# Performance work log

Hardware: AMD Instinct MI355X
Metric: run time of the kernel (lower is better)

The kernel has to match this reference:

```python
import jax, jax.numpy as jnp
import numpy as np

N, F, F1 = 8192, 256, 64
EDGE_PROB = 0.01  # adjacency density


def setup_inputs() -> dict:
    key = jax.random.key(0)
    kX, kA, kW, ka = jax.random.split(key, 4)
    X = jax.random.normal(kX, (N, F), dtype=jnp.float32)
    # binary adjacency mask (float, as in the original where A multiplies the -1e10 mask)
    A = (jax.random.uniform(kA, (N, N)) < EDGE_PROB).astype(jnp.float32)
    # glorot_uniform init for W [F1, F] and a [2, F1, 1]
    limW = float(np.sqrt(6.0 / (F1 + F)))
    W = jax.random.uniform(kW, (F1, F), minval=-limW, maxval=limW, dtype=jnp.float32)
    lima = float(np.sqrt(6.0 / (F1 + 1)))
    a = jax.random.uniform(ka, (2, F1, 1), minval=-lima, maxval=lima, dtype=jnp.float32)
    return {"X": X, "A": A, "W": W, "a": a}


def reference(X, A, W, a):
    x_features = X @ W.T                       # [N, F1]
    att_self = x_features @ a[0]               # [N, 1]
    att_neighbours = x_features @ a[1]         # [N, 1]
    att = att_self + att_neighbours.T          # [N, N] broadcast additive score
    att = jnp.where(att > 0, att, 0.2 * att)   # LeakyReLU(alpha=0.2)
    att_masked = att + (-1e10) * (1.0 - A)     # mask non-edges
    dense = jax.nn.softmax(att_masked, axis=0) # column-wise softmax (axis=0, as in source)
    return dense @ x_features                  # [N, F1]
```

## Files before the change

kernel.cpp:

```cpp
#include <hip/hip_runtime.h>
#include <math.h>

#define NN   8192
#define FF   256
#define FF1  64
#define CAP  256
#define RREP 32

__global__ __launch_bounds__(256) void k1_feat(const float* __restrict__ X,
                                               const float* __restrict__ W,
                                               const float* __restrict__ a,
                                               float* __restrict__ xf,
                                               float* __restrict__ s,
                                               float* __restrict__ t,
                                               float* __restrict__ D_rep) {
    __shared__ float Xs[32 * FF];
    const int tid  = threadIdx.x;
    const int row0 = blockIdx.x * 32;

    {
        const int gid = blockIdx.x * 256 + tid;
        ((float4*)D_rep)[gid] = make_float4(0.f, 0.f, 0.f, 0.f);
    }

    const float4* Xg  = (const float4*)(X + (size_t)row0 * FF);
    float4*       Xs4 = (float4*)Xs;
#pragma unroll
    for (int v = 0; v < 8; ++v) Xs4[tid + v * 256] = Xg[tid + v * 256];
    __syncthreads();

    const int f  = tid & 63;
    const int rg = tid >> 6;

    float acc[8] = {0.f,0.f,0.f,0.f,0.f,0.f,0.f,0.f};
    const float4* Wrow = (const float4*)(W + (size_t)f * FF);
    for (int k4 = 0; k4 < FF / 4; ++k4) {
        float4 wv = Wrow[k4];
#pragma unroll
        for (int r = 0; r < 8; ++r) {
            float4 xv = *(const float4*)&Xs[(rg * 8 + r) * FF + k4 * 4];
            acc[r] = fmaf(wv.x, xv.x, acc[r]);
            acc[r] = fmaf(wv.y, xv.y, acc[r]);
            acc[r] = fmaf(wv.z, xv.z, acc[r]);
            acc[r] = fmaf(wv.w, xv.w, acc[r]);
        }
    }

    const float a0 = a[f];
    const float a1 = a[FF1 + f];
#pragma unroll
    for (int r = 0; r < 8; ++r) {
        const int row = row0 + rg * 8 + r;
        xf[(size_t)row * FF1 + f] = acc[r];
        float vs = acc[r] * a0;
        float vt = acc[r] * a1;
#pragma unroll
        for (int off = 32; off; off >>= 1) {
            vs += __shfl_xor(vs, off);
            vt += __shfl_xor(vt, off);
        }
        if (f == 0) { s[row] = vs; t[row] = vt; }
    }
}

__global__ __launch_bounds__(256) void k2_scan(const float* __restrict__ A,
                                               unsigned short* __restrict__ idx,
                                               int* __restrict__ counts) {
    const int tid  = threadIdx.x;
    const int lane = tid & 63;
    const int wv   = tid >> 6;
    __shared__ unsigned short lbuf[256 * 8];
    __shared__ int wtot[4];

    for (int r = 0; r < 4; ++r) {
        const int i = blockIdx.x * 4 + r;
        int c = 0;
        const float4* Arow = (const float4*)(A + (size_t)i * NN);
#pragma unroll
        for (int k = 0; k < 8; ++k) {
            const int v = tid + k * 256;
            float4 av = Arow[v];
            if (av.x != 0.f) { lbuf[tid * 8 + (c & 7)] = (unsigned short)(4 * v + 0); ++c; }
            if (av.y != 0.f) { lbuf[tid * 8 + (c & 7)] = (unsigned short)(4 * v + 1); ++c; }
            if (av.z != 0.f) { lbuf[tid * 8 + (c & 7)] = (unsigned short)(4 * v + 2); ++c; }
            if (av.w != 0.f) { lbuf[tid * 8 + (c & 7)] = (unsigned short)(4 * v + 3); ++c; }
        }
        if (c > 8) c = 8;

        int sc = c;
#pragma unroll
        for (int off = 1; off < 64; off <<= 1) {
            int n = __shfl_up(sc, off);
            if (lane >= off) sc += n;
        }
        if (lane == 63) wtot[wv] = sc;
        __syncthreads();

        int base = sc - c;
#pragma unroll
        for (int w = 0; w < 4; ++w) if (w < wv) base += wtot[w];

        for (int q = 0; q < c; ++q) {
            const int pos = base + q;
            if (pos < CAP) idx[(size_t)i * CAP + pos] = lbuf[tid * 8 + q];
        }
        if (tid == 255) {
            const int total = base + c;
            counts[i] = (total < CAP) ? total : CAP;
        }
        __syncthreads();
    }
}

__global__ __launch_bounds__(256) void k2b_edge(const float* __restrict__ s,
                                                const float* __restrict__ t,
                                                const unsigned short* __restrict__ idx,
                                                const int* __restrict__ counts,
                                                float* __restrict__ ev,
                                                float* __restrict__ D_rep) {
    const int wv   = threadIdx.x >> 6;
    const int lane = threadIdx.x & 63;
    const int i    = blockIdx.x * 4 + wv;
    float* __restrict__ Dr = D_rep + (size_t)(blockIdx.x & (RREP - 1)) * NN;

    const int   cnt = counts[i];
    const float si  = s[i];
    for (int p = lane; p < cnt; p += 64) {
        const int j = idx[(size_t)i * CAP + p];
        const float x  = si + t[j];
        const float lr = x > 0.f ? x : 0.2f * x;
        const float e  = __expf(lr);
        ev[(size_t)i * CAP + p] = e;
        unsafeAtomicAdd(&Dr[j], e);
    }
}

__global__ __launch_bounds__(256) void k2c_yf(const float* __restrict__ D_rep,
                                              const float* __restrict__ xf,
                                              float* __restrict__ yf) {
    const int wv   = threadIdx.x >> 6;
    const int lane = threadIdx.x & 63;
    const int j    = blockIdx.x * 4 + wv;

    float d = (lane < RREP) ? D_rep[(size_t)lane * NN + j] : 0.f;
#pragma unroll
    for (int off = 16; off; off >>= 1) d += __shfl_xor(d, off);
    d = __shfl(d, 0);
    const float rD = 1.0f / d;
    yf[(size_t)j * FF1 + lane] = xf[(size_t)j * FF1 + lane] * rD;
}

__global__ __launch_bounds__(256) void k3_apply(const float* __restrict__ yf,
                                                const unsigned short* __restrict__ idx,
                                                const float* __restrict__ ev,
                                                const int* __restrict__ counts,
                                                float* __restrict__ out) {
    const int wave = threadIdx.x >> 6;
    const int lane = threadIdx.x & 63;
    const int i    = blockIdx.x * 4 + wave;

    const int cnt = counts[i];
    float acc0 = 0.f, acc1 = 0.f, acc2 = 0.f, acc3 = 0.f;

    for (int base = 0; base < cnt; base += 64) {
        const int p = base + lane;
        const bool act = (p < cnt);
        int   j = act ? (int)idx[(size_t)i * CAP + p] : 0;
        float w = act ? ev[(size_t)i * CAP + p] : 0.f;

#pragma unroll
        for (int e = 0; e < 64; e += 4) {
            {
                const int   je = __builtin_amdgcn_readlane(j, e + 0);
                const float we = __int_as_float(__builtin_amdgcn_readlane(__float_as_int(w), e + 0));
                acc0 = fmaf(we, yf[(size_t)je * FF1 + lane], acc0);
            }
            {
                const int   je = __builtin_amdgcn_readlane(j, e + 1);
                const float we = __int_as_float(__builtin_amdgcn_readlane(__float_as_int(w), e + 1));
                acc1 = fmaf(we, yf[(size_t)je * FF1 + lane], acc1);
            }
            {
                const int   je = __builtin_amdgcn_readlane(j, e + 2);
                const float we = __int_as_float(__builtin_amdgcn_readlane(__float_as_int(w), e + 2));
                acc2 = fmaf(we, yf[(size_t)je * FF1 + lane], acc2);
            }
            {
                const int   je = __builtin_amdgcn_readlane(j, e + 3);
                const float we = __int_as_float(__builtin_amdgcn_readlane(__float_as_int(w), e + 3));
                acc3 = fmaf(we, yf[(size_t)je * FF1 + lane], acc3);
            }
        }
    }
    out[(size_t)i * FF1 + lane] = (acc0 + acc1) + (acc2 + acc3);
}

extern "C" void kernel_launch(void* const* d_in, const int* in_sizes, int n_in,
                              void* d_out, int out_size, void* d_ws, size_t ws_size,
                              hipStream_t stream) {
    const float* X = (const float*)d_in[0];
    const float* A = (const float*)d_in[1];
    const float* W = (const float*)d_in[2];
    const float* a = (const float*)d_in[3];
    float* out = (float*)d_out;

    char* ws = (char*)d_ws;
    float* xf = (float*)ws;                                  ws += (size_t)NN * FF1 * 4;
    float* yf = (float*)ws;                                  ws += (size_t)NN * FF1 * 4;
    float* s  = (float*)ws;                                  ws += (size_t)NN * 4;
    float* t  = (float*)ws;                                  ws += (size_t)NN * 4;
    int*   counts = (int*)ws;                                ws += (size_t)NN * 4;
    unsigned short* idx = (unsigned short*)ws;               ws += (size_t)NN * CAP * 2;
    float* ev = (float*)ws;                                  ws += (size_t)NN * CAP * 4;
    float* D_rep = (float*)ws;

    k1_feat<<<NN / 32, 256, 0, stream>>>(X, W, a, xf, s, t, D_rep);
    k2_scan<<<NN / 4, 256, 0, stream>>>(A, idx, counts);
    k2b_edge<<<NN / 4, 256, 0, stream>>>(s, t, idx, counts, ev, D_rep);
    k2c_yf<<<NN / 4, 256, 0, stream>>>(D_rep, xf, yf);
    k3_apply<<<NN / 4, 256, 0, stream>>>(yf, idx, ev, counts, out);
}
```

Before: 109.7 us.

## Merge feature GEMM and adjacency scan into one heterogeneous launch; skip empty chunks

Combines the X@W feature kernel and the adjacency-row scan into a single launch whose blocks branch by blockIdx. The feature part is re-tiled to 8 rows per block (1024 blocks) so it can run alongside the bandwidth-bound scan blocks. This removes one launch and the serialization between two independent stages. The apply kernel also skips 16-edge readlane chunks beyond the neighbour count, avoiding wasted gathers from padded lanes. The merged kernel carries the shared-memory footprint of both paths and has lower register reuse per feature row.

After: 119.6 us. +9.0%, slower.

```diff
diff --git a/kernel.cpp b/kernel.cpp
--- a/kernel.cpp
+++ b/kernel.cpp
@@ -6,109 +6,103 @@
 #define FF1  64
 #define CAP  256
 #define RREP 32
-
-__global__ __launch_bounds__(256) void k1_feat(const float* __restrict__ X,
-                                               const float* __restrict__ W,
-                                               const float* __restrict__ a,
-                                               float* __restrict__ xf,
-                                               float* __restrict__ s,
-                                               float* __restrict__ t,
-                                               float* __restrict__ D_rep) {
-    __shared__ float Xs[32 * FF];
-    const int tid  = threadIdx.x;
-    const int row0 = blockIdx.x * 32;
-
-    {
-        const int gid = blockIdx.x * 256 + tid;
-        ((float4*)D_rep)[gid] = make_float4(0.f, 0.f, 0.f, 0.f);
-    }
-
-    const float4* Xg  = (const float4*)(X + (size_t)row0 * FF);
-    float4*       Xs4 = (float4*)Xs;
-#pragma unroll
-    for (int v = 0; v < 8; ++v) Xs4[tid + v * 256] = Xg[tid + v * 256];
-    __syncthreads();
-
-    const int f  = tid & 63;
-    const int rg = tid >> 6;
-
-    float acc[8] = {0.f,0.f,0.f,0.f,0.f,0.f,0.f,0.f};
-    const float4* Wrow = (const float4*)(W + (size_t)f * FF);
-    for (int k4 = 0; k4 < FF / 4; ++k4) {
-        float4 wv = Wrow[k4];
-#pragma unroll
-        for (int r = 0; r < 8; ++r) {
-            float4 xv = *(const float4*)&Xs[(rg * 8 + r) * FF + k4 * 4];
-            acc[r] = fmaf(wv.x, xv.x, acc[r]);
-            acc[r] = fmaf(wv.y, xv.y, acc[r]);
-            acc[r] = fmaf(wv.z, xv.z, acc[r]);
-            acc[r] = fmaf(wv.w, xv.w, acc[r]);
-        }
-    }
-
-    const float a0 = a[f];
-    const float a1 = a[FF1 + f];
-#pragma unroll
-    for (int r = 0; r < 8; ++r) {
-        const int row = row0 + rg * 8 + r;
-        xf[(size_t)row * FF1 + f] = acc[r];
-        float vs = acc[r] * a0;
-        float vt = acc[r] * a1;
-#pragma unroll
-        for (int off = 32; off; off >>= 1) {
-            vs += __shfl_xor(vs, off);
-            vt += __shfl_xor(vt, off);
-        }
-        if (f == 0) { s[row] = vs; t[row] = vt; }
-    }
-}
-
-__global__ __launch_bounds__(256) void k2_scan(const float* __restrict__ A,
-                                               unsigned short* __restrict__ idx,
-                                               int* __restrict__ counts) {
+#define K1B  1024
+#define SCB  2048
+
+__global__ __launch_bounds__(256) void kA(const float* __restrict__ X,
+                                          const float* __restrict__ A,
+                                          const float* __restrict__ W,
+                                          const float* __restrict__ a,
+                                          float* __restrict__ xf,
+                                          float* __restrict__ s,
+                                          float* __restrict__ t,
+                                          float* __restrict__ D_rep,
+                                          unsigned short* __restrict__ idx,
+                                          int* __restrict__ counts) {
+    __shared__ float          Xs[8 * FF];
+    __shared__ unsigned short lbuf[256 * 8];
+    __shared__ int            wtot[4];
+
     const int tid  = threadIdx.x;
     const int lane = tid & 63;
     const int wv   = tid >> 6;
-    __shared__ unsigned short lbuf[256 * 8];
-    __shared__ int wtot[4];
-
-    for (int r = 0; r < 4; ++r) {
-        const int i = blockIdx.x * 4 + r;
-        int c = 0;
-        const float4* Arow = (const float4*)(A + (size_t)i * NN);
-#pragma unroll
-        for (int k = 0; k < 8; ++k) {
-            const int v = tid + k * 256;
-            float4 av = Arow[v];
-            if (av.x != 0.f) { lbuf[tid * 8 + (c & 7)] = (unsigned short)(4 * v + 0); ++c; }
-            if (av.y != 0.f) { lbuf[tid * 8 + (c & 7)] = (unsigned short)(4 * v + 1); ++c; }
-            if (av.z != 0.f) { lbuf[tid * 8 + (c & 7)] = (unsigned short)(4 * v + 2); ++c; }
-            if (av.w != 0.f) { lbuf[tid * 8 + (c & 7)] = (unsigned short)(4 * v + 3); ++c; }
-        }
-        if (c > 8) c = 8;
-
-        int sc = c;
-#pragma unroll
-        for (int off = 1; off < 64; off <<= 1) {
-            int n = __shfl_up(sc, off);
-            if (lane >= off) sc += n;
-        }
-        if (lane == 63) wtot[wv] = sc;
+
+    if (blockIdx.x < K1B) {
+        const int row0 = blockIdx.x * 8;
+
+        const int gid = blockIdx.x * 256 + tid;
+        if (gid < RREP * NN / 4) ((float4*)D_rep)[gid] = make_float4(0.f,0.f,0.f,0.f);
+
+        const float4* Xg  = (const float4*)(X + (size_t)row0 * FF);
+        float4* Xs4 = (float4*)Xs;
+        Xs4[tid]       = Xg[tid];
+        Xs4[tid + 256] = Xg[tid + 256];
         __syncthreads();
 
-        int base = sc - c;
-#pragma unroll
-        for (int w = 0; w < 4; ++w) if (w < wv) base += wtot[w];
-
-        for (int q = 0; q < c; ++q) {
-            const int pos = base + q;
-            if (pos < CAP) idx[(size_t)i * CAP + pos] = lbuf[tid * 8 + q];
-        }
-        if (tid == 255) {
-            const int total = base + c;
-            counts[i] = (total < CAP) ? total : CAP;
-        }
-        __syncthreads();
+        const int f  = lane;
+        const int r0 = wv * 2;
+        float acc0 = 0.f, acc1 = 0.f;
+        const float4* Wrow = (const float4*)(W + (size_t)f * FF);
+        for (int k4 = 0; k4 < FF / 4; ++k4) {
+            const float4 wq = Wrow[k4];
+            const float4 x0 = *(const float4*)&Xs[r0 * FF + k4 * 4];
+            const float4 x1 = *(const float4*)&Xs[(r0 + 1) * FF + k4 * 4];
+            acc0 = fmaf(wq.x, x0.x, acc0); acc0 = fmaf(wq.y, x0.y, acc0);
+            acc0 = fmaf(wq.z, x0.z, acc0); acc0 = fmaf(wq.w, x0.w, acc0);
+            acc1 = fmaf(wq.x, x1.x, acc1); acc1 = fmaf(wq.y, x1.y, acc1);
+            acc1 = fmaf(wq.z, x1.z, acc1); acc1 = fmaf(wq.w, x1.w, acc1);
+        }
+        const float a0 = a[f], a1 = a[FF1 + f];
+        xf[(size_t)(row0 + r0) * FF1 + f]     = acc0;
+        xf[(size_t)(row0 + r0 + 1) * FF1 + f] = acc1;
+        float vs0 = acc0 * a0, vt0 = acc0 * a1;
+        float vs1 = acc1 * a0, vt1 = acc1 * a1;
+#pragma unroll
+        for (int off = 32; off; off >>= 1) {
+            vs0 += __shfl_xor(vs0, off); vt0 += __shfl_xor(vt0, off);
+            vs1 += __shfl_xor(vs1, off); vt1 += __shfl_xor(vt1, off);
+        }
+        if (lane == 0) {
+            s[row0 + r0] = vs0; s[row0 + r0 + 1] = vs1;
+            t[row0 + r0] = vt0; t[row0 + r0 + 1] = vt1;
+        }
+    } else {
+        const int sb = blockIdx.x - K1B;
+        for (int r = 0; r < 4; ++r) {
+            const int i = sb * 4 + r;
+            int c = 0;
+            const float4* Arow = (const float4*)(A + (size_t)i * NN);
+#pragma unroll
+            for (int k = 0; k < 8; ++k) {
+                const int v = tid + k * 256;
+                float4 av = Arow[v];
+                if (av.x != 0.f) { lbuf[tid * 8 + (c & 7)] = (unsigned short)(4 * v + 0); ++c; }
+                if (av.y != 0.f) { lbuf[tid * 8 + (c & 7)] = (unsigned short)(4 * v + 1); ++c; }
+                if (av.z != 0.f) { lbuf[tid * 8 + (c & 7)] = (unsigned short)(4 * v + 2); ++c; }
+                if (av.w != 0.f) { lbuf[tid * 8 + (c & 7)] = (unsigned short)(4 * v + 3); ++c; }
+            }
+            if (c > 8) c = 8;
+
+            int sc = c;
+#pragma unroll
+            for (int off = 1; off < 64; off <<= 1) {
+                int n = __shfl_up(sc, off);
+                if (lane >= off) sc += n;
+            }
+            if (lane == 63) wtot[wv] = sc;
+            __syncthreads();
+
+            int base = sc - c;
+#pragma unroll
+            for (int w = 0; w < 4; ++w) if (w < wv) base += wtot[w];
+
+            for (int q = 0; q < c; ++q) {
+                const int pos = base + q;
+                if (pos < CAP) idx[(size_t)i * CAP + pos] = lbuf[tid * 8 + q];
+            }
+            if (tid == 255) counts[i] = (base + c < CAP) ? (base + c) : CAP;
+            __syncthreads();
+        }
     }
 }
 
@@ -146,8 +140,7 @@
 #pragma unroll
     for (int off = 16; off; off >>= 1) d += __shfl_xor(d, off);
     d = __shfl(d, 0);
-    const float rD = 1.0f / d;
-    yf[(size_t)j * FF1 + lane] = xf[(size_t)j * FF1 + lane] * rD;
+    yf[(size_t)j * FF1 + lane] = xf[(size_t)j * FF1 + lane] * (1.0f / d);
 }
 
 __global__ __launch_bounds__(256) void k3_apply(const float* __restrict__ yf,
@@ -165,30 +158,27 @@
     for (int base = 0; base < cnt; base += 64) {
         const int p = base + lane;
         const bool act = (p < cnt);
-        int   j = act ? (int)idx[(size_t)i * CAP + p] : 0;
-        float w = act ? ev[(size_t)i * CAP + p] : 0.f;
-
-#pragma unroll
-        for (int e = 0; e < 64; e += 4) {
-            {
-                const int   je = __builtin_amdgcn_readlane(j, e + 0);
-                const float we = __int_as_float(__builtin_amdgcn_readlane(__float_as_int(w), e + 0));
-                acc0 = fmaf(we, yf[(size_t)je * FF1 + lane], acc0);
-            }
-            {
-                const int   je = __builtin_amdgcn_readlane(j, e + 1);
-                const float we = __int_as_float(__builtin_amdgcn_readlane(__float_as_int(w), e + 1));
-                acc1 = fmaf(we, yf[(size_t)je * FF1 + lane], acc1);
-            }
-            {
-                const int   je = __builtin_amdgcn_readlane(j, e + 2);
-                const float we = __int_as_float(__builtin_amdgcn_readlane(__float_as_int(w), e + 2));
-                acc2 = fmaf(we, yf[(size_t)je * FF1 + lane], acc2);
-            }
-            {
-                const int   je = __builtin_amdgcn_readlane(j, e + 3);
-                const float we = __int_as_float(__builtin_amdgcn_readlane(__float_as_int(w), e + 3));
-                acc3 = fmaf(we, yf[(size_t)je * FF1 + lane], acc3);
+        int   jj = act ? (int)idx[(size_t)i * CAP + p] : 0;
+        float ww = act ? ev[(size_t)i * CAP + p] : 0.f;
+
+#pragma unroll
+        for (int eb = 0; eb < 64; eb += 16) {
+            if (base + eb < cnt) {
+#pragma unroll
+                for (int e = eb; e < eb + 16; e += 4) {
+                    { const int je = __builtin_amdgcn_readlane(jj, e + 0);
+                      const float we = __int_as_float(__builtin_amdgcn_readlane(__float_as_int(ww), e + 0));
+                      acc0 = fmaf(we, yf[(size_t)je * FF1 + lane], acc0); }
+                    { const int je = __builtin_amdgcn_readlane(jj, e + 1);
+                      const float we = __int_as_float(__builtin_amdgcn_readlane(__float_as_int(ww), e + 1));
+                      acc1 = fmaf(we, yf[(size_t)je * FF1 + lane], acc1); }
+                    { const int je = __builtin_amdgcn_readlane(jj, e + 2);
+                      const float we = __int_as_float(__builtin_amdgcn_readlane(__float_as_int(ww), e + 2));
+                      acc2 = fmaf(we, yf[(size_t)je * FF1 + lane], acc2); }
+                    { const int je = __builtin_amdgcn_readlane(jj, e + 3);
+                      const float we = __int_as_float(__builtin_amdgcn_readlane(__float_as_int(ww), e + 3));
+                      acc3 = fmaf(we, yf[(size_t)je * FF1 + lane], acc3); }
+                }
             }
         }
     }
@@ -214,8 +204,7 @@
     float* ev = (float*)ws;                                  ws += (size_t)NN * CAP * 4;
     float* D_rep = (float*)ws;
 
-    k1_feat<<<NN / 32, 256, 0, stream>>>(X, W, a, xf, s, t, D_rep);
-    k2_scan<<<NN / 4, 256, 0, stream>>>(A, idx, counts);
+    kA<<<K1B + SCB, 256, 0, stream>>>(X, A, W, a, xf, s, t, D_rep, idx, counts);
     k2b_edge<<<NN / 4, 256, 0, stream>>>(s, t, idx, counts, ev, D_rep);
     k2c_yf<<<NN / 4, 256, 0, stream>>>(D_rep, xf, yf);
     k3_apply<<<NN / 4, 256, 0, stream>>>(yf, idx, ev, counts, out);
```
